# Kernel tuning notes

Hardware: AMD Instinct MI355X
Metric: run time of the kernel (lower is better)

The kernel has to match this reference:

```python
import jax, jax.numpy as jnp
import numpy as np

N_NODES = 50000
ELU_ALPHA = 0.2  # torch.nn.ELU(0.2): alpha=0.2


def _elu(v, alpha):
    return jnp.where(v > 0, v, alpha * jnp.expm1(v))


def setup_inputs() -> dict:
    key = jax.random.key(0)
    k1, k2, k3, k4, k5 = jax.random.split(key, 5)
    fin, H, F = 128, 4, 32
    E = 1600000
    return {
        "x": jax.random.normal(k1, (N_NODES, fin), dtype=jnp.float32),
        "W": jax.random.normal(k2, (fin, H * F), dtype=jnp.float32) * (1.414 / np.sqrt(fin)),
        "a_src": jax.random.normal(k3, (H, F), dtype=jnp.float32) * 0.1,
        "a_tgt": jax.random.normal(k4, (H, F), dtype=jnp.float32) * 0.1,
        "edge_index": jax.random.randint(k5, (E, 2), 0, N_NODES, dtype=jnp.int64),
    }


def reference(x, W, a_src, a_tgt, edge_index):
    # GAT layer (dropout omitted: eval mode). x: [N, fin]
    N = x.shape[0]
    H, F = a_src.shape
    xp = (x @ W).reshape(N, H, F)                 # projected node feats [N,H,F]
    s_src = jnp.einsum("nhf,hf->nh", xp, a_src)   # per-head source scores [N,H]
    s_tgt = jnp.einsum("nhf,hf->nh", xp, a_tgt)   # per-head target scores [N,H]

    src = edge_index[:, 0]
    tgt = edge_index[:, 1]

    # edge-wise gather (the memory-bound hotspot)
    e = _elu(s_src[src] + s_tgt[tgt], ELU_ALPHA)  # [E,H]

    # segment softmax over edges sharing a target node
    m = jax.ops.segment_max(e, tgt, num_segments=N)           # [N,H]
    m = jnp.where(jnp.isfinite(m), m, 0.0)
    ex = jnp.exp(e - m[tgt])                                  # [E,H]
    denom = jax.ops.segment_sum(ex, tgt, num_segments=N)      # [N,H]
    alpha = ex / denom[tgt]                                   # [E,H]

    # gather source features, weight, scatter-add into target nodes
    msg = alpha[:, :, None] * xp[src]                          # [E,H,F]
    out = jax.ops.segment_sum(msg, tgt, num_segments=N)        # [N,H,F]
    return out.reshape(N, H * F)                               # concat heads
```

## Files before the change

### kernel.cpp

```cpp
#include <hip/hip_runtime.h>
#include <hip/hip_bf16.h>
#include <math.h>

#define FIN 128
#define NHEAD 4
#define CH 128
#define ELU_A 0.2f

#define BSHIFT 8
#define NB 196
#define CAP 16384
#define T_EDGES 2048

typedef unsigned int uint32;

__device__ __forceinline__ float bf16lo(uint32 u) {
    union { uint32 i; float f; } c; c.i = u << 16; return c.f;
}
__device__ __forceinline__ float bf16hi(uint32 u) {
    union { uint32 i; float f; } c; c.i = u & 0xffff0000u; return c.f;
}

__global__ __launch_bounds__(256) void gemm_scores_kernel(
    const float* __restrict__ x, const float* __restrict__ W,
    const float* __restrict__ a_src, const float* __restrict__ a_tgt,
    __hip_bfloat16* __restrict__ xpb, float* __restrict__ s_src,
    float* __restrict__ s_tgt, int N)
{
    __shared__ float sx[32 * FIN];
    const int t = threadIdx.x;
    const int row0 = blockIdx.x * 32;

    for (int i = t * 4; i < 32 * FIN; i += 256 * 4) {
        int r = row0 + (i >> 7);
        if (r < N)
            *(float4*)&sx[i] = *(const float4*)&x[(size_t)r * FIN + (i & 127)];
    }
    __syncthreads();

    const int tc = t & 31;
    const int tr = t >> 5;
    const float4* sx4 = (const float4*)sx;
    const float4* W4  = (const float4*)W;

    float acc[4][4] = {};
    for (int k4 = 0; k4 < FIN / 4; ++k4) {
        float4 wv0 = W4[(k4 * 4 + 0) * 32 + tc];
        float4 wv1 = W4[(k4 * 4 + 1) * 32 + tc];
        float4 wv2 = W4[(k4 * 4 + 2) * 32 + tc];
        float4 wv3 = W4[(k4 * 4 + 3) * 32 + tc];
#pragma unroll
        for (int i = 0; i < 4; ++i) {
            float4 xv = sx4[(tr * 4 + i) * 32 + k4];
            acc[i][0] += xv.x * wv0.x + xv.y * wv1.x + xv.z * wv2.x + xv.w * wv3.x;
            acc[i][1] += xv.x * wv0.y + xv.y * wv1.y + xv.z * wv2.y + xv.w * wv3.y;
            acc[i][2] += xv.x * wv0.z + xv.y * wv1.z + xv.z * wv2.z + xv.w * wv3.z;
            acc[i][3] += xv.x * wv0.w + xv.y * wv1.w + xv.z * wv2.w + xv.w * wv3.w;
        }
    }

#pragma unroll
    for (int i = 0; i < 4; ++i) {
        int r = row0 + tr * 4 + i;
        if (r < N) {
            __hip_bfloat16 o[4];
            o[0] = __float2bfloat16(acc[i][0]);
            o[1] = __float2bfloat16(acc[i][1]);
            o[2] = __float2bfloat16(acc[i][2]);
            o[3] = __float2bfloat16(acc[i][3]);
            *(uint2*)&xpb[(size_t)r * CH + tc * 4] = *(const uint2*)o;
        }
    }

    float4 asv = *(const float4*)&a_src[tc * 4];
    float4 atv = *(const float4*)&a_tgt[tc * 4];
#pragma unroll
    for (int i = 0; i < 4; ++i) {
        float ps = acc[i][0] * asv.x + acc[i][1] * asv.y + acc[i][2] * asv.z + acc[i][3] * asv.w;
        float pt = acc[i][0] * atv.x + acc[i][1] * atv.y + acc[i][2] * atv.z + acc[i][3] * atv.w;
#pragma unroll
        for (int off = 1; off < 8; off <<= 1) {
            ps += __shfl_xor(ps, off);
            pt += __shfl_xor(pt, off);
        }
        int r = row0 + tr * 4 + i;
        if ((tc & 7) == 0 && r < N) {
            int h = tc >> 3;
            s_src[(size_t)r * NHEAD + h] = ps;
            s_tgt[(size_t)r * NHEAD + h] = pt;
        }
    }
}

__global__ __launch_bounds__(256) void partition_kernel(
    const int2* __restrict__ ei2, int* __restrict__ bcnt,
    uint32* __restrict__ ebuck, int E)
{
    __shared__ uint32 stage[T_EDGES];
    __shared__ int hist[256], scanbuf[256], loff[256], cnt2[256], base[256];
    const int tid = threadIdx.x;
    const int e0 = blockIdx.x * T_EDGES;
    const int tile = min(T_EDGES, E - e0);

    hist[tid] = 0; cnt2[tid] = 0;
    __syncthreads();

    uint32 rec[8];
#pragma unroll
    for (int j = 0; j < 8; ++j) {
        int idx = e0 + j * 256 + tid;
        if (idx < E) {
            int2 p = ei2[idx];
            rec[j] = (uint32)p.x | ((uint32)p.y << 16);
            atomicAdd(&hist[p.y >> BSHIFT], 1);
        } else rec[j] = 0xFFFFFFFFu;
    }
    __syncthreads();

    scanbuf[tid] = hist[tid];
    __syncthreads();
    for (int off = 1; off < 256; off <<= 1) {
        int v = (tid >= off) ? scanbuf[tid - off] : 0;
        __syncthreads();
        scanbuf[tid] += v;
        __syncthreads();
    }
    loff[tid] = scanbuf[tid] - hist[tid];
    if (tid < NB && hist[tid] > 0)
        base[tid] = tid * CAP + atomicAdd(&bcnt[tid], hist[tid]);
    __syncthreads();

#pragma unroll
    for (int j = 0; j < 8; ++j) {
        if (rec[j] != 0xFFFFFFFFu) {
            int b = rec[j] >> (16 + BSHIFT);
            int r = atomicAdd(&cnt2[b], 1);
            stage[loff[b] + r] = rec[j];
        }
    }
    __syncthreads();

    for (int i = tid; i < tile; i += 256) {
        uint32 rc = stage[i];
        int b = rc >> (16 + BSHIFT);
        ebuck[(size_t)base[b] + (i - loff[b])] = rc;
    }
}

__global__ __launch_bounds__(256) void bscan_kernel(
    const int* __restrict__ bcnt, int* __restrict__ bbase)
{
    __shared__ int s[256];
    const int t = threadIdx.x;
    int v = (t < NB) ? bcnt[t] : 0;
    s[t] = v;
    __syncthreads();
    for (int off = 1; off < 256; off <<= 1) {
        int u = (t >= off) ? s[t - off] : 0;
        __syncthreads();
        s[t] += u;
        __syncthreads();
    }
    if (t < NB) bbase[t] = s[t] - v;
}

__global__ __launch_bounds__(1024) void fine_scatter_kernel(
    const uint32* __restrict__ ebuck, const int* __restrict__ bcnt,
    const int* __restrict__ bbase, int* __restrict__ deg,
    int* __restrict__ rowptr, int* __restrict__ srcs, int N)
{
    __shared__ int ldeg[256], psum[256], lcur[256];
    const int b = blockIdx.x;
    const int tid = threadIdx.x;
    if (tid < 256) ldeg[tid] = 0;
    __syncthreads();

    const int cnt = bcnt[b];
    const uint32* rp = ebuck + (size_t)b * CAP;

    for (int i = tid; i < cnt; i += 1024)
        atomicAdd(&ldeg[(rp[i] >> 16) & 255], 1);
    __syncthreads();

    if (tid < 256) psum[tid] = ldeg[tid];
    __syncthreads();
    for (int off = 1; off < 256; off <<= 1) {
        int u = 0;
        if (tid < 256 && tid >= off) u = psum[tid - off];
        __syncthreads();
        if (tid < 256) psum[tid] += u;
        __syncthreads();
    }

    const int gb = bbase[b];
    if (tid < 256) {
        int pref = gb + psum[tid] - ldeg[tid];
        lcur[tid] = pref;
        int node = b * 256 + tid;
        if (node < N) { deg[node] = ldeg[tid]; rowptr[node] = pref; }
    }
    __syncthreads();

    for (int i = tid; i < cnt; i += 1024) {
        uint32 rc = rp[i];
        int pos = atomicAdd(&lcur[(rc >> 16) & 255], 1);
        srcs[pos] = rc & 0xffff;
    }
}

__global__ __launch_bounds__(256) void aggregate_kernel(
    const int* __restrict__ srcs, const int* __restrict__ rowptr,
    const int* __restrict__ deg, const float* __restrict__ s_src,
    const float* __restrict__ s_tgt, const uint32* __restrict__ xpb,
    float* __restrict__ out, int N)
{
    const int lane = threadIdx.x & 63;
    const int wid  = __builtin_amdgcn_readfirstlane(threadIdx.x >> 6);
    const int t = blockIdx.x * 4 + wid;
    if (t >= N) return;

    const int start = __builtin_amdgcn_readfirstlane(rowptr[t]);
    const int d     = __builtin_amdgcn_readfirstlane(deg[t]);
    const int h     = lane >> 4;
    const int cj    = lane & 7;
    const int chh   = (lane >> 3) & 3;

    const float st_c = s_tgt[(size_t)t * NHEAD + chh];
    const float st_h = s_tgt[(size_t)t * NHEAD + h];
    const int bb = h * 8;

    float accx = 0.0f, accy = 0.0f, dsum = 0.0f;
    int k = 0;

    for (; k + 8 <= d; k += 8) {
        int   sv = srcs[start + k + cj];
        float a  = s_src[(size_t)sv * NHEAD + chh];
        float v  = a + st_c;
        float u  = v > 0.0f ? v : ELU_A * (__expf(v) - 1.0f);
        float e  = __expf(u);

        int s0 = srcs[start + k + 0], s1 = srcs[start + k + 1];
        int s2 = srcs[start + k + 2], s3 = srcs[start + k + 3];
        int s4 = srcs[start + k + 4], s5 = srcs[start + k + 5];
        int s6 = srcs[start + k + 6], s7 = srcs[start + k + 7];

        uint32 x0 = xpb[(size_t)s0 * 64 + lane];
        uint32 x1 = xpb[(size_t)s1 * 64 + lane];
        uint32 x2 = xpb[(size_t)s2 * 64 + lane];
        uint32 x3 = xpb[(size_t)s3 * 64 + lane];
        uint32 x4 = xpb[(size_t)s4 * 64 + lane];
        uint32 x5 = xpb[(size_t)s5 * 64 + lane];
        uint32 x6 = xpb[(size_t)s6 * 64 + lane];
        uint32 x7 = xpb[(size_t)s7 * 64 + lane];

        float e0 = __shfl(e, bb + 0), e1 = __shfl(e, bb + 1);
        float e2 = __shfl(e, bb + 2), e3 = __shfl(e, bb + 3);
        float e4 = __shfl(e, bb + 4), e5 = __shfl(e, bb + 5);
        float e6 = __shfl(e, bb + 6), e7 = __shfl(e, bb + 7);

#define ACC(E, X) { dsum += (E); accx += (E) * bf16lo(X); accy += (E) * bf16hi(X); }
        ACC(e0, x0) ACC(e1, x1) ACC(e2, x2) ACC(e3, x3)
        ACC(e4, x4) ACC(e5, x5) ACC(e6, x6) ACC(e7, x7)
#undef ACC
    }

    for (; k < d; ++k) {
        int   s  = srcs[start + k];
        float a  = s_src[(size_t)s * NHEAD + h];
        uint32 xv = xpb[(size_t)s * 64 + lane];
        float v = a + st_h;
        float u = v > 0.0f ? v : ELU_A * (__expf(v) - 1.0f);
        float e = __expf(u);
        dsum += e; accx += e * bf16lo(xv); accy += e * bf16hi(xv);
    }

    float inv = (d > 0) ? 1.0f / dsum : 0.0f;
    float2 o = make_float2(accx * inv, accy * inv);
    *(float2*)&out[(size_t)t * CH + lane * 2] = o;
}

extern "C" void kernel_launch(void* const* d_in, const int* in_sizes, int n_in,
                              void* d_out, int out_size, void* d_ws, size_t ws_size,
                              hipStream_t stream)
{
    const float* x     = (const float*)d_in[0];
    const float* W     = (const float*)d_in[1];
    const float* a_src = (const float*)d_in[2];
    const float* a_tgt = (const float*)d_in[3];
    const int*   ei    = (const int*)d_in[4];

    const int N = in_sizes[0] / FIN;
    const int E = in_sizes[4] / 2;

    char* ws = (char*)d_ws;
    __hip_bfloat16* xpb = (__hip_bfloat16*)ws;  ws += (size_t)N * CH * sizeof(__hip_bfloat16);
    float* s_src  = (float*)ws;                 ws += (size_t)N * NHEAD * sizeof(float);
    float* s_tgt  = (float*)ws;                 ws += (size_t)N * NHEAD * sizeof(float);
    int*   deg    = (int*)ws;                   ws += (size_t)N * sizeof(int);
    int*   bcnt   = (int*)ws;                   ws += (size_t)NB * sizeof(int);
    int*   bbase  = (int*)ws;                   ws += (size_t)NB * sizeof(int);
    int*   rowptr = (int*)ws;                   ws += (size_t)N * sizeof(int);
    int*   srcs   = (int*)ws;                   ws += (size_t)E * sizeof(int);
    uint32* ebuck = (uint32*)ws;                ws += (size_t)NB * CAP * sizeof(uint32);

    float* out = (float*)d_out;
    const int2* ei2 = (const int2*)ei;

    hipMemsetAsync(bcnt, 0, (size_t)NB * sizeof(int), stream);

    partition_kernel<<<(E + T_EDGES - 1) / T_EDGES, 256, 0, stream>>>(
        ei2, bcnt, ebuck, E);
    bscan_kernel<<<1, 256, 0, stream>>>(bcnt, bbase);
    fine_scatter_kernel<<<NB, 1024, 0, stream>>>(
        ebuck, bcnt, bbase, deg, rowptr, srcs, N);

    gemm_scores_kernel<<<(N + 31) / 32, 256, 0, stream>>>(
        x, W, a_src, a_tgt, xpb, s_src, s_tgt, N);

    aggregate_kernel<<<(N + 3) / 4, 256, 0, stream>>>(
        srcs, rowptr, deg, s_src, s_tgt, (const uint32*)xpb, out, N);
}
```

Measured before the change: 141.5 us.

## Replace FP32 projection GEMM with bf16 MFMA kernel and separate score pass

The scalar FP32 x@W projection is replaced by a bf16 MFMA 16x16x32 kernel. A one-block prep kernel transposes W and converts it to bf16, and the x rows are converted to bf16 in registers. Attention scores are now computed in their own kernel from the bf16-rounded projected features rather than from the FP32 accumulators. This cuts ALU cost of the GEMM, but adds two launches and an extra read of xp, and the scores now carry bf16 rounding of both x and xp.

Result: faster. 133.5 us (-5.7%).

```diff
diff --git a/kernel.cpp b/kernel.cpp
--- a/kernel.cpp
+++ b/kernel.cpp
@@ -13,6 +13,8 @@
 #define T_EDGES 2048
 
 typedef unsigned int uint32;
+typedef __attribute__((ext_vector_type(8))) short short8;
+typedef __attribute__((ext_vector_type(4))) float f32x4;
 
 __device__ __forceinline__ float bf16lo(uint32 u) {
     union { uint32 i; float f; } c; c.i = u << 16; return c.f;
@@ -20,75 +22,108 @@
 __device__ __forceinline__ float bf16hi(uint32 u) {
     union { uint32 i; float f; } c; c.i = u & 0xffff0000u; return c.f;
 }
-
-__global__ __launch_bounds__(256) void gemm_scores_kernel(
-    const float* __restrict__ x, const float* __restrict__ W,
-    const float* __restrict__ a_src, const float* __restrict__ a_tgt,
-    __hip_bfloat16* __restrict__ xpb, float* __restrict__ s_src,
+__device__ __forceinline__ unsigned short f2b(float f) {
+    union { float f; uint32 u; } c; c.f = f;
+    uint32 u = c.u;
+    return (unsigned short)((u + 0x7fffu + ((u >> 16) & 1u)) >> 16);
+}
+
+__global__ __launch_bounds__(256) void wprep_kernel(
+    const float* __restrict__ W, unsigned short* __restrict__ Wt)
+{
+    __shared__ float w[FIN * CH];
+    for (int i = threadIdx.x; i < FIN * CH; i += 256) w[i] = W[i];
+    __syncthreads();
+    const int n  = threadIdx.x >> 1;
+    const int kh = (threadIdx.x & 1) * 64;
+    for (int kb = 0; kb < 64; kb += 8) {
+        unsigned short v[8];
+#pragma unroll
+        for (int j = 0; j < 8; ++j) v[j] = f2b(w[(kh + kb + j) * CH + n]);
+        *(uint4*)&Wt[(size_t)n * FIN + kh + kb] = *(uint4*)v;
+    }
+}
+
+__global__ __launch_bounds__(256) void gemm_mfma_kernel(
+    const float* __restrict__ x, const unsigned short* __restrict__ Wt,
+    unsigned short* __restrict__ xpb, int N)
+{
+    __shared__ unsigned short cbuf[4][16][132];
+    const int lane = threadIdx.x & 63;
+    const int wid  = threadIdx.x >> 6;
+    const int rowbase = blockIdx.x * 64 + wid * 16;
+
+    const int rr   = min(rowbase + (lane & 15), N - 1);
+    const int krow = (lane >> 4) * 8;
+
+    f32x4 acc[8];
+#pragma unroll
+    for (int c = 0; c < 8; ++c) acc[c] = (f32x4){0.f, 0.f, 0.f, 0.f};
+
+#pragma unroll
+    for (int s = 0; s < 4; ++s) {
+        const int koff = s * 32 + krow;
+        const float* xr = x + (size_t)rr * FIN + koff;
+        float4 p0 = *(const float4*)xr;
+        float4 p1 = *(const float4*)(xr + 4);
+        short8 af;
+        af[0] = (short)f2b(p0.x); af[1] = (short)f2b(p0.y);
+        af[2] = (short)f2b(p0.z); af[3] = (short)f2b(p0.w);
+        af[4] = (short)f2b(p1.x); af[5] = (short)f2b(p1.y);
+        af[6] = (short)f2b(p1.z); af[7] = (short)f2b(p1.w);
+#pragma unroll
+        for (int c = 0; c < 8; ++c) {
+            const short8 bf = *(const short8*)&Wt[(size_t)(c * 16 + (lane & 15)) * FIN + koff];
+            acc[c] = __builtin_amdgcn_mfma_f32_16x16x32_bf16(af, bf, acc[c], 0, 0, 0);
+        }
+    }
+
+#pragma unroll
+    for (int c = 0; c < 8; ++c)
+#pragma unroll
+        for (int r = 0; r < 4; ++r)
+            cbuf[wid][(lane >> 4) * 4 + r][c * 16 + (lane & 15)] = f2b(acc[c][r]);
+    __syncthreads();
+
+    for (int r = 0; r < 16; ++r) {
+        int row = rowbase + r;
+        if (row < N) {
+            uint32 v = *(const uint32*)&cbuf[wid][r][lane * 2];
+            *(uint32*)&xpb[(size_t)row * CH + lane * 2] = v;
+        }
+    }
+}
+
+__global__ __launch_bounds__(256) void scores_kernel(
+    const uint32* __restrict__ xpb, const float* __restrict__ a_src,
+    const float* __restrict__ a_tgt, float* __restrict__ s_src,
     float* __restrict__ s_tgt, int N)
 {
-    __shared__ float sx[32 * FIN];
     const int t = threadIdx.x;
-    const int row0 = blockIdx.x * 32;
-
-    for (int i = t * 4; i < 32 * FIN; i += 256 * 4) {
-        int r = row0 + (i >> 7);
-        if (r < N)
-            *(float4*)&sx[i] = *(const float4*)&x[(size_t)r * FIN + (i & 127)];
-    }
-    __syncthreads();
-
-    const int tc = t & 31;
-    const int tr = t >> 5;
-    const float4* sx4 = (const float4*)sx;
-    const float4* W4  = (const float4*)W;
-
-    float acc[4][4] = {};
-    for (int k4 = 0; k4 < FIN / 4; ++k4) {
-        float4 wv0 = W4[(k4 * 4 + 0) * 32 + tc];
-        float4 wv1 = W4[(k4 * 4 + 1) * 32 + tc];
-        float4 wv2 = W4[(k4 * 4 + 2) * 32 + tc];
-        float4 wv3 = W4[(k4 * 4 + 3) * 32 + tc];
-#pragma unroll
-        for (int i = 0; i < 4; ++i) {
-            float4 xv = sx4[(tr * 4 + i) * 32 + k4];
-            acc[i][0] += xv.x * wv0.x + xv.y * wv1.x + xv.z * wv2.x + xv.w * wv3.x;
-            acc[i][1] += xv.x * wv0.y + xv.y * wv1.y + xv.z * wv2.y + xv.w * wv3.y;
-            acc[i][2] += xv.x * wv0.z + xv.y * wv1.z + xv.z * wv2.z + xv.w * wv3.z;
-            acc[i][3] += xv.x * wv0.w + xv.y * wv1.w + xv.z * wv2.w + xv.w * wv3.w;
-        }
-    }
-
-#pragma unroll
-    for (int i = 0; i < 4; ++i) {
-        int r = row0 + tr * 4 + i;
-        if (r < N) {
-            __hip_bfloat16 o[4];
-            o[0] = __float2bfloat16(acc[i][0]);
-            o[1] = __float2bfloat16(acc[i][1]);
-            o[2] = __float2bfloat16(acc[i][2]);
-            o[3] = __float2bfloat16(acc[i][3]);
-            *(uint2*)&xpb[(size_t)r * CH + tc * 4] = *(const uint2*)o;
-        }
-    }
-
-    float4 asv = *(const float4*)&a_src[tc * 4];
-    float4 atv = *(const float4*)&a_tgt[tc * 4];
-#pragma unroll
-    for (int i = 0; i < 4; ++i) {
-        float ps = acc[i][0] * asv.x + acc[i][1] * asv.y + acc[i][2] * asv.z + acc[i][3] * asv.w;
-        float pt = acc[i][0] * atv.x + acc[i][1] * atv.y + acc[i][2] * atv.z + acc[i][3] * atv.w;
-#pragma unroll
-        for (int off = 1; off < 8; off <<= 1) {
-            ps += __shfl_xor(ps, off);
-            pt += __shfl_xor(pt, off);
-        }
-        int r = row0 + tr * 4 + i;
-        if ((tc & 7) == 0 && r < N) {
-            int h = tc >> 3;
-            s_src[(size_t)r * NHEAD + h] = ps;
-            s_tgt[(size_t)r * NHEAD + h] = pt;
-        }
+    const int n = blockIdx.x * 16 + (t >> 4);
+    const int g = t & 15;
+    if (n >= N) return;
+
+    uint4 xv = *(const uint4*)&xpb[(size_t)n * 64 + g * 4];
+    float xs[8] = { bf16lo(xv.x), bf16hi(xv.x), bf16lo(xv.y), bf16hi(xv.y),
+                    bf16lo(xv.z), bf16hi(xv.z), bf16lo(xv.w), bf16hi(xv.w) };
+    float4 as0 = *(const float4*)&a_src[g * 8];
+    float4 as1 = *(const float4*)&a_src[g * 8 + 4];
+    float4 at0 = *(const float4*)&a_tgt[g * 8];
+    float4 at1 = *(const float4*)&a_tgt[g * 8 + 4];
+
+    float ps = xs[0]*as0.x + xs[1]*as0.y + xs[2]*as0.z + xs[3]*as0.w
+             + xs[4]*as1.x + xs[5]*as1.y + xs[6]*as1.z + xs[7]*as1.w;
+    float pt = xs[0]*at0.x + xs[1]*at0.y + xs[2]*at0.z + xs[3]*at0.w
+             + xs[4]*at1.x + xs[5]*at1.y + xs[6]*at1.z + xs[7]*at1.w;
+
+    ps += __shfl_xor(ps, 1); ps += __shfl_xor(ps, 2);
+    pt += __shfl_xor(pt, 1); pt += __shfl_xor(pt, 2);
+
+    if ((g & 3) == 0) {
+        int h = g >> 2;
+        s_src[(size_t)n * NHEAD + h] = ps;
+        s_tgt[(size_t)n * NHEAD + h] = pt;
     }
 }
 
@@ -293,7 +328,8 @@
     const int E = in_sizes[4] / 2;
 
     char* ws = (char*)d_ws;
-    __hip_bfloat16* xpb = (__hip_bfloat16*)ws;  ws += (size_t)N * CH * sizeof(__hip_bfloat16);
+    unsigned short* xpb = (unsigned short*)ws;  ws += (size_t)N * CH * sizeof(unsigned short);
+    unsigned short* Wt  = (unsigned short*)ws;  ws += (size_t)FIN * CH * sizeof(unsigned short);
     float* s_src  = (float*)ws;                 ws += (size_t)N * NHEAD * sizeof(float);
     float* s_tgt  = (float*)ws;                 ws += (size_t)N * NHEAD * sizeof(float);
     int*   deg    = (int*)ws;                   ws += (size_t)N * sizeof(int);
@@ -308,14 +344,16 @@
 
     hipMemsetAsync(bcnt, 0, (size_t)NB * sizeof(int), stream);
 
+    wprep_kernel<<<1, 256, 0, stream>>>(W, Wt);
     partition_kernel<<<(E + T_EDGES - 1) / T_EDGES, 256, 0, stream>>>(
         ei2, bcnt, ebuck, E);
     bscan_kernel<<<1, 256, 0, stream>>>(bcnt, bbase);
     fine_scatter_kernel<<<NB, 1024, 0, stream>>>(
         ebuck, bcnt, bbase, deg, rowptr, srcs, N);
 
-    gemm_scores_kernel<<<(N + 31) / 32, 256, 0, stream>>>(
-        x, W, a_src, a_tgt, xpb, s_src, s_tgt, N);
+    gemm_mfma_kernel<<<(N + 63) / 64, 256, 0, stream>>>(x, Wt, xpb, N);
+    scores_kernel<<<(N + 15) / 16, 256, 0, stream>>>(
+        (const uint32*)xpb, a_src, a_tgt, s_src, s_tgt, N);
 
     aggregate_kernel<<<(N + 3) / 4, 256, 0, stream>>>(
         srcs, rowptr, deg, s_src, s_tgt, (const uint32*)xpb, out, N);
```
